# Performance work log

Measured on AMD Instinct MI355X. Metric: run time of the kernel, lower is better.

The kernel has to match this reference:

```python
import jax, jax.numpy as jnp
from jax import lax
import numpy as np

H = W = 768
N_BOXES = 512
C1, C2 = 32, 64
POOL = 5
NUM_CLASSES = 4
BN_EPS = 1e-5


def setup_inputs() -> dict:
    key = jax.random.key(0)
    ks = jax.random.split(key, 20)
    image = jax.random.normal(ks[0], (1, 3, H, W), jnp.float32)
    # valid boxes: xmax>xmin, ymax>ymin, inside [0, W)
    xmin = jax.random.randint(ks[1], (N_BOXES,), 0, W - 256)
    ymin = jax.random.randint(ks[2], (N_BOXES,), 0, H - 256)
    bw = jax.random.randint(ks[3], (N_BOXES,), 8, 256)
    bh = jax.random.randint(ks[4], (N_BOXES,), 8, 256)
    boxes = jnp.stack([xmin, ymin, xmin + bw, ymin + bh], axis=1).astype(jnp.int32)
    conv1_w = jax.random.normal(ks[5], (C1, 3, 3, 3), jnp.float32) * 0.1
    conv1_b = jax.random.normal(ks[6], (C1,), jnp.float32) * 0.01
    bn1_g = 1.0 + 0.1 * jax.random.normal(ks[7], (C1,), jnp.float32)
    bn1_b = 0.1 * jax.random.normal(ks[8], (C1,), jnp.float32)
    bn1_m = 0.1 * jax.random.normal(ks[9], (C1,), jnp.float32)
    bn1_v = jax.random.uniform(ks[10], (C1,), jnp.float32, 0.5, 1.5)
    conv2_w = jax.random.normal(ks[11], (C2, C1, 3, 3), jnp.float32) * 0.05
    conv2_b = jax.random.normal(ks[12], (C2,), jnp.float32) * 0.01
    bn2_g = 1.0 + 0.1 * jax.random.normal(ks[13], (C2,), jnp.float32)
    bn2_b = 0.1 * jax.random.normal(ks[14], (C2,), jnp.float32)
    bn2_m = 0.1 * jax.random.normal(ks[15], (C2,), jnp.float32)
    bn2_v = jax.random.uniform(ks[16], (C2,), jnp.float32, 0.5, 1.5)
    fc1_w = jax.random.normal(ks[17], (128, C2 * POOL * POOL), jnp.float32) * 0.02
    fc1_b = jnp.zeros((128,), jnp.float32)
    fc2_w = jax.random.normal(ks[18], (NUM_CLASSES, 128), jnp.float32) * 0.05
    fc2_b = jnp.zeros((NUM_CLASSES,), jnp.float32)
    return dict(image=image, boxes=boxes,
                conv1_w=conv1_w, conv1_b=conv1_b, bn1_g=bn1_g, bn1_b=bn1_b, bn1_m=bn1_m, bn1_v=bn1_v,
                conv2_w=conv2_w, conv2_b=conv2_b, bn2_g=bn2_g, bn2_b=bn2_b, bn2_m=bn2_m, bn2_v=bn2_v,
                fc1_w=fc1_w, fc1_b=fc1_b, fc2_w=fc2_w, fc2_b=fc2_b)


def _conv(x, w, b):
    y = lax.conv_general_dilated(x, w, (1, 1), ((1, 1), (1, 1)),
                                 dimension_numbers=("NCHW", "OIHW", "NCHW"))
    return y + b[None, :, None, None]


def _bn(x, g, b, m, v):
    scale = g / jnp.sqrt(v + BN_EPS)
    return x * scale[None, :, None, None] + (b - m * scale)[None, :, None, None]


def _forward(image, boxes, conv1_w, conv1_b, bn1_g, bn1_b, bn1_m, bn1_v,
             conv2_w, conv2_b, bn2_g, bn2_b, bn2_m, bn2_v,
             fc1_w, fc1_b, fc2_w, fc2_b):
    # backbone: Conv -> ReLU -> BN (order as in source), twice
    x = _bn(jax.nn.relu(_conv(image, conv1_w, conv1_b)), bn1_g, bn1_b, bn1_m, bn1_v)
    x = _bn(jax.nn.relu(_conv(x, conv2_w, conv2_b)), bn2_g, bn2_b, bn2_m, bn2_v)
    feat = x[0]  # [C2, H, W], batch assumed 1 as in the per-box slicing loop
    # integral image for exact adaptive-avg-pool over integer index rectangles
    integ = jnp.pad(feat, ((0, 0), (1, 0), (1, 0))).cumsum(1).cumsum(2)  # [C2,H+1,W+1]
    xmin, ymin, xmax, ymax = boxes[:, 0], boxes[:, 1], boxes[:, 2], boxes[:, 3]
    bh = ymax - ymin
    bw = xmax - xmin
    i = jnp.arange(POOL)
    # AdaptiveAvgPool2d bin edges: start=floor(i*L/5), end=ceil((i+1)*L/5)
    y0 = ymin[:, None] + (i * bh[:, None]) // POOL            # [N,5]
    y1 = ymin[:, None] + ((i + 1) * bh[:, None] + POOL - 1) // POOL
    x0 = xmin[:, None] + (i * bw[:, None]) // POOL
    x1 = xmin[:, None] + ((i + 1) * bw[:, None] + POOL - 1) // POOL

    def rect(ys, xs):  # [C2, N, 5, 5]
        return integ[:, ys[:, :, None], xs[:, None, :]]

    s = rect(y1, x1) - rect(y0, x1) - rect(y1, x0) + rect(y0, x0)
    area = ((y1 - y0)[:, :, None] * (x1 - x0)[:, None, :]).astype(feat.dtype)  # [N,5,5]
    pooled = s / area[None]                                    # [C2,N,5,5]
    flat = pooled.transpose(1, 0, 2, 3).reshape(boxes.shape[0], -1)  # [N, C2*25]
    h1 = jax.nn.relu(flat @ fc1_w.T + fc1_b)  # dropout is identity in eval
    return h1 @ fc2_w.T + fc2_b               # [N, num_classes]


def reference(image, boxes, conv1_w, conv1_b, bn1_g, bn1_b, bn1_m, bn1_v,
              conv2_w, conv2_b, bn2_g, bn2_b, bn2_m, bn2_v,
              fc1_w, fc1_b, fc2_w, fc2_b):
    return _forward(image, boxes, conv1_w, conv1_b, bn1_g, bn1_b, bn1_m, bn1_v,
                    conv2_w, conv2_b, bn2_g, bn2_b, bn2_m, bn2_v,
                    fc1_w, fc1_b, fc2_w, fc2_b)
```

## Files before the change

### kernel.cpp

```cpp
#include <hip/hip_runtime.h>
#include <hip/hip_bf16.h>

#define HH 768
#define WW 768
#define HWSZ (HH*WW)
#define BN_EPS 1e-5f
#define SEG 12
#define NSEG 64

typedef __attribute__((ext_vector_type(8))) short bf16x8;
typedef __attribute__((ext_vector_type(4))) float f32x4;

__device__ __forceinline__ float bf2f(unsigned short u) {
  union { unsigned int i; float f; } v; v.i = ((unsigned int)u) << 16; return v.f;
}
__device__ __forceinline__ unsigned short f2bf(float f) {
  union { float f; unsigned int i; } v; v.f = f;
  unsigned int x = v.i;
  return (unsigned short)((x + 0x7fffu + ((x >> 16) & 1u)) >> 16);
}
__device__ __forceinline__ float ldf(const void* p, int i, int flag) {
  return flag ? bf2f(((const unsigned short*)p)[i]) : ((const float*)p)[i];
}

#define DPP_ADD(v, CTRL) do {                                              \
    union { float f; int i; } _u; _u.f = (v);                              \
    int _t = __builtin_amdgcn_update_dpp(0, _u.i, (CTRL), 0xf, 0xf, true); \
    union { int i; float f; } _w; _w.i = _t;                               \
    (v) += _w.f;                                                           \
  } while (0)
__device__ __forceinline__ float row_prefix16(float v) {
  DPP_ADD(v, 0x111);
  DPP_ADD(v, 0x112);
  DPP_ADD(v, 0x114);
  DPP_ADD(v, 0x118);
  return v;
}

__global__ void k_prep(const void* __restrict__ c1b,
                       const void* __restrict__ g1, const void* __restrict__ b1,
                       const void* __restrict__ m1, const void* __restrict__ v1,
                       const void* __restrict__ c2b, const void* __restrict__ g2,
                       const void* __restrict__ b2, const void* __restrict__ m2,
                       const void* __restrict__ v2, const void* __restrict__ w1,
                       const void* __restrict__ fb1, const void* __restrict__ fw2,
                       const void* __restrict__ fb2,
                       int* __restrict__ flagp, float* __restrict__ cst)
{
  __shared__ int sflag;
  int tid = threadIdx.x;
  if (tid == 0) {
    const unsigned short* v1raw = (const unsigned short*)v1;
    int ok = 1;
    #pragma unroll
    for (int j = 0; j < 4; ++j) {
      unsigned short u = v1raw[2*j];
      if (u < 0x3E00u || u > 0x4040u) ok = 0;
    }
    sflag = ok;
    *flagp = ok;
  }
  __syncthreads();
  int flag = sflag;
  float* wc1   = cst;
  float* bias1 = cst + 864;
  float* sc1   = cst + 896;
  float* sh1   = cst + 928;
  float* bias2 = cst + 960;
  float* sc2   = cst + 1024;
  float* sh2   = cst + 1088;
  float* fb1c  = cst + 1152;
  float* w2c   = cst + 1280;
  float* fb2c  = cst + 1792;
  if (tid < 32) {
    float s = ldf(g1, tid, flag) * rsqrtf(ldf(v1, tid, flag) + BN_EPS);
    sc1[tid] = s;
    sh1[tid] = ldf(b1, tid, flag) - ldf(m1, tid, flag) * s;
    bias1[tid] = ldf(c1b, tid, flag);
  }
  if (tid < 64) {
    float s = ldf(g2, tid, flag) * rsqrtf(ldf(v2, tid, flag) + BN_EPS);
    sc2[tid] = s;
    sh2[tid] = ldf(b2, tid, flag) - ldf(m2, tid, flag) * s;
    bias2[tid] = ldf(c2b, tid, flag);
  }
  if (tid < 128) fb1c[tid] = ldf(fb1, tid, flag);
  if (tid < 4)   fb2c[tid] = ldf(fb2, tid, flag);
  for (int i = tid; i < 512; i += 256) w2c[i] = ldf(fw2, i, flag);
  for (int idx = tid; idx < 27*32; idx += 256) {
    int k = idx >> 5, co = idx & 31;
    wc1[idx] = ldf(w1, co*27 + k, flag);
  }
}

__global__ void k_a2(const void* __restrict__ w2, const int* __restrict__ flagp,
                     unsigned short* __restrict__ A2)
{
  int flag = *flagp;
  int idx = blockIdx.x * 256 + threadIdx.x;
  if (idx < 80*288) {
    int o = idx / 288, k = idx % 288, tap = k >> 5, ci = k & 31;
    A2[idx] = (o < 64) ? f2bf(ldf(w2, (o*32 + ci)*9 + tap, flag)) : (unsigned short)0;
  }
}

__global__ void k_cvtw1(unsigned short* __restrict__ dst, const void* __restrict__ src,
                        const int* __restrict__ flagp) {
  int flag = *flagp;
  for (int i = blockIdx.x * blockDim.x + threadIdx.x; i < 128*1600;
       i += gridDim.x * blockDim.x) {
    int t = i / 1600, r = i % 1600, cell = r >> 6, c = r & 63;
    dst[i] = f2bf(ldf(src, t*1600 + c*25 + cell, flag));
  }
}

__global__ __launch_bounds__(256) void k_conv1(const void* __restrict__ img,
    const int* __restrict__ flagp, const float* __restrict__ cst,
    unsigned short* __restrict__ feat1)
{
  const float* wc1   = cst;
  const float* bias1 = cst + 864;
  const float* sc1   = cst + 896;
  const float* sh1   = cst + 928;
  int flag = *flagp;
  __shared__ float tile[3][18][18];
  int tx = threadIdx.x, ty = threadIdx.y;
  int tid = ty * 16 + tx;
  int x0 = blockIdx.x * 16, y0 = blockIdx.y * 16;
  for (int idx = tid; idx < 3*18*18; idx += 256) {
    int ci = idx / 324, rem = idx % 324, r = rem / 18, cc = rem % 18;
    int gy = y0 - 1 + r, gx = x0 - 1 + cc;
    float v = 0.f;
    if (gy >= 0 && gy < HH && gx >= 0 && gx < WW)
      v = ldf(img, ci*HWSZ + gy*WW + gx, flag);
    tile[ci][r][cc] = v;
  }
  __syncthreads();
  float acc[32];
  #pragma unroll
  for (int c = 0; c < 32; ++c) acc[c] = 0.f;
  #pragma unroll
  for (int ci = 0; ci < 3; ++ci)
    #pragma unroll
    for (int ky = 0; ky < 3; ++ky)
      #pragma unroll
      for (int kx = 0; kx < 3; ++kx) {
        float v = tile[ci][ty + ky][tx + kx];
        const float* wr = wc1 + (ci*9 + ky*3 + kx) * 32;
        #pragma unroll
        for (int c = 0; c < 32; ++c) acc[c] += v * wr[c];
      }
  int gy = y0 + ty, gx = x0 + tx;
  unsigned short* dst = feat1 + (gy*WW + gx) * 32;
  #pragma unroll
  for (int g = 0; g < 4; ++g) {
    bf16x8 pack;
    #pragma unroll
    for (int e = 0; e < 8; ++e) {
      int c = g*8 + e;
      float r = fmaxf(acc[c] + bias1[c], 0.f);
      float f = r * sc1[c] + sh1[c];
      pack[e] = (short)f2bf(f);
    }
    *(bf16x8*)(dst + g*8) = pack;
  }
}

__global__ __launch_bounds__(256) void k_conv2t(const unsigned short* __restrict__ feat1,
    const unsigned short* __restrict__ A2, const float* __restrict__ cst,
    float* __restrict__ T)
{
  const float* bias2 = cst + 960;
  const float* sc2   = cst + 1024;
  const float* sh2   = cst + 1088;
  __shared__ unsigned short tile[14 * 34 * 40];
  int tid = threadIdx.x;
  int xb = blockIdx.x, ys = blockIdx.y;
  int x0 = xb * 32, ybase = ys * SEG;

  for (int idx = tid; idx < 14*34*4; idx += 256) {
    int q = idx & 3, p = (idx >> 2) % 34, r = idx / 136;
    int gy = ybase - 1 + r, gx = x0 - 1 + p;
    uint4 val = make_uint4(0u, 0u, 0u, 0u);
    if (gy >= 0 && gy < HH && gx >= 0 && gx < WW)
      val = *(const uint4*)(feat1 + (gy*WW + gx)*32 + q*8);
    *(uint4*)(tile + (r*34 + p)*40 + q*8) = val;
  }

  int w = tid >> 6, lane = tid & 63, quad = lane >> 4, l16 = lane & 15;
  int m = w * 16 + l16;
  bf16x8 afrag[9];
  #pragma unroll
  for (int t = 0; t < 9; ++t)
    afrag[t] = *(const bf16x8*)(A2 + m*288 + t*32 + quad*8);
  float bs[4], scv[4], shv[4];
  #pragma unroll
  for (int r = 0; r < 4; ++r) {
    int c = w*16 + quad*4 + r;
    bs[r] = bias2[c]; scv[r] = sc2[c]; shv[r] = sh2[c];
  }
  __syncthreads();

  f32x4 ys0 = (f32x4){0.f,0.f,0.f,0.f};
  f32x4 ys1 = (f32x4){0.f,0.f,0.f,0.f};
  int cbase = w*16 + quad*4;
  for (int dy = 0; dy < SEG; ++dy) {
    int y = ybase + dy;
    f32x4 acc[2];
    acc[0] = (f32x4){0.f,0.f,0.f,0.f};
    acc[1] = (f32x4){0.f,0.f,0.f,0.f};
    #pragma unroll
    for (int t = 0; t < 9; ++t) {
      int ky = t / 3, kx = t % 3;
      #pragma unroll
      for (int i = 0; i < 2; ++i) {
        int px = i*16 + l16 + kx;
        bf16x8 b = *(const bf16x8*)(tile + ((dy + ky)*34 + px)*40 + quad*8);
        acc[i] = __builtin_amdgcn_mfma_f32_16x16x32_bf16(afrag[t], b, acc[i], 0, 0, 0);
      }
    }
    #pragma unroll
    for (int r = 0; r < 4; ++r) {
      float v0 = fmaxf(acc[0][r] + bs[r], 0.f) * scv[r] + shv[r];
      float v1 = fmaxf(acc[1][r] + bs[r], 0.f) * scv[r] + shv[r];
      v0 = row_prefix16(v0);
      v1 = row_prefix16(v1);
      v1 += __shfl(v0, 15, 16);
      ys0[r] += v0;
      ys1[r] += v1;
    }
    *(f32x4*)(T + ((size_t)(y*WW + x0 + l16))*64 + cbase)      = ys0;
    *(f32x4*)(T + ((size_t)(y*WW + x0 + 16 + l16))*64 + cbase) = ys1;
  }
}

__global__ __launch_bounds__(64) void k_cgen_i(const float* __restrict__ T,
                                               float* __restrict__ C)
{
  int j = blockIdx.x, c = threadIdx.x;
  float run = 0.f;
  for (int i = 0; i < NSEG; ++i) {
    run += T[((size_t)((i*SEG + SEG-1)*WW + j*32 + 31))*64 + c];
    C[((size_t)(i*24 + j))*64 + c] = run;
  }
}
__global__ __launch_bounds__(64) void k_cgen_j(float* __restrict__ C)
{
  int i = blockIdx.x, c = threadIdx.x;
  float run = 0.f;
  #pragma unroll
  for (int j = 0; j < 24; ++j) {
    size_t idx = ((size_t)(i*24 + j))*64 + c;
    run += C[idx];
    C[idx] = run;
  }
}

__global__ __launch_bounds__(256) void k_ab(const float* __restrict__ T,
    const float* __restrict__ C, float* __restrict__ A, float* __restrict__ Bp)
{
  int part = blockIdx.y, tid = threadIdx.x;
  int c = tid & 63, s = tid >> 6;
  if (part == 0) {
    int y = blockIdx.x * 4 + s;
    float run = 0.f;
    #pragma unroll
    for (int j = 0; j < 24; ++j) {
      run += T[((size_t)(y*WW + j*32 + 31))*64 + c];
      A[((size_t)(y*24 + j))*64 + c] = run;
    }
  } else {
    int x = blockIdx.x * 4 + s;
    int j = x >> 5;
    float run = 0.f;
    for (int i = 0; i < NSEG; ++i) {
      run += T[((size_t)((i*SEG + SEG-1)*WW + x))*64 + c];
      float cj = (j > 0) ? C[((size_t)(i*24 + (j-1)))*64 + c] : 0.f;
      Bp[((size_t)(i*WW + x))*64 + c] = run + cj;
    }
  }
}

__device__ __forceinline__ float icorner(const float* __restrict__ T,
    const float* __restrict__ A, const float* __restrict__ Bp,
    int c, int yy, int xx)
{
  int i = yy / SEG, j = xx >> 5;
  float v = T[((size_t)(yy*WW + xx))*64 + c];
  if (j > 0) v += A[((size_t)(yy*24 + (j-1)))*64 + c];
  if (i > 0) v += Bp[((size_t)((i-1)*WW + xx))*64 + c];
  return v;
}

__global__ __launch_bounds__(256) void k_roi3(const float* __restrict__ T,
    const float* __restrict__ A, const float* __restrict__ Bp,
    const int* __restrict__ boxes, float* __restrict__ flat)
{
  int b = blockIdx.x;
  int xmin = boxes[b*4 + 0], ymin = boxes[b*4 + 1];
  int xmax = boxes[b*4 + 2], ymax = boxes[b*4 + 3];
  int bh = ymax - ymin, bw = xmax - xmin;
  for (int idx = threadIdx.x; idx < 1600; idx += 256) {
    int c = idx & 63, cell = idx >> 6, i = cell / 5, j = cell % 5;
    int y0 = ymin + (i*bh)/5,  y1 = ymin + ((i+1)*bh + 4)/5;
    int x0 = xmin + (j*bw)/5,  x1 = xmin + ((j+1)*bw + 4)/5;
    float s = icorner(T, A, Bp, c, y1-1, x1-1);
    if (y0 > 0)           s -= icorner(T, A, Bp, c, y0-1, x1-1);
    if (x0 > 0)           s -= icorner(T, A, Bp, c, y1-1, x0-1);
    if (y0 > 0 && x0 > 0) s += icorner(T, A, Bp, c, y0-1, x0-1);
    float area = (float)((y1 - y0) * (x1 - x0));
    flat[b*1600 + cell*64 + c] = s / area;
  }
}

__global__ __launch_bounds__(256) void k_conv2_c16(const unsigned short* __restrict__ feat1,
    const unsigned short* __restrict__ A2, const float* __restrict__ cst,
    float* __restrict__ chunk, int c0, int cnw)
{
  const float* bias2 = cst + 960;
  const float* sc2   = cst + 1024;
  const float* sh2   = cst + 1088;
  __shared__ unsigned short tile[3 * 130 * 40];
  int tid = threadIdx.x;
  int y = blockIdx.y, x0 = blockIdx.x * 128;
  for (int idx = tid; idx < 3*130*4; idx += 256) {
    int q = idx & 3, p = (idx >> 2) % 130, r = idx / 520;
    int gy = y - 1 + r, gx = x0 - 1 + p;
    uint4 val = make_uint4(0u, 0u, 0u, 0u);
    if (gy >= 0 && gy < HH && gx >= 0 && gx < WW)
      val = *(const uint4*)(feat1 + (gy*WW + gx)*32 + q*8);
    *(uint4*)(tile + (r*130 + p)*40 + q*8) = val;
  }
  __syncthreads();
  int w = tid >> 6, lane = tid & 63, quad = lane >> 4, l16 = lane & 15;
  int m = c0 + l16;
  f32x4 acc[2];
  acc[0] = (f32x4){0.f,0.f,0.f,0.f};
  acc[1] = (f32x4){0.f,0.f,0.f,0.f};
  #pragma unroll
  for (int t = 0; t < 9; ++t) {
    int ky = t / 3, kx = t % 3;
    bf16x8 a = *(const bf16x8*)(A2 + m*288 + t*32 + quad*8);
    #pragma unroll
    for (int i = 0; i < 2; ++i) {
      int px = w*32 + i*16 + l16 + kx;
      bf16x8 b = *(const bf16x8*)(tile + (ky*130 + px)*40 + quad*8);
      acc[i] = __builtin_amdgcn_mfma_f32_16x16x32_bf16(a, b, acc[i], 0, 0, 0);
    }
  }
  #pragma unroll
  for (int r = 0; r < 4; ++r) {
    int cl = quad*4 + r;
    if (cl < cnw) {
      int c = c0 + cl;
      float bsv = bias2[c], s = sc2[c], sh = sh2[c];
      float* dst = chunk + cl*HWSZ + y*WW;
      #pragma unroll
      for (int i = 0; i < 2; ++i) {
        float v = fmaxf(acc[i][r] + bsv, 0.f) * s + sh;
        dst[x0 + w*32 + i*16 + l16] = v;
      }
    }
  }
}
__global__ __launch_bounds__(256) void k_csy(float* __restrict__ buf) {
  int t = blockIdx.x * 256 + threadIdx.x;
  int c = t / WW, x = t % WW;
  float* p = buf + c*HWSZ + x;
  float run = 0.f;
  for (int yb = 0; yb < HH; yb += 16) {
    float v[16];
    #pragma unroll
    for (int j = 0; j < 16; ++j) v[j] = p[(yb + j) * WW];
    #pragma unroll
    for (int j = 0; j < 16; ++j) { run += v[j]; v[j] = run; }
    #pragma unroll
    for (int j = 0; j < 16; ++j) p[(yb + j) * WW] = v[j];
  }
}
__global__ __launch_bounds__(256) void k_csx(float* __restrict__ buf) {
  int row = blockIdx.x * 4 + (threadIdx.x >> 6);
  int lane = threadIdx.x & 63;
  float* p = buf + (long)row * WW;
  float carry = 0.f;
  for (int ch = 0; ch < 12; ++ch) {
    float v = p[ch*64 + lane];
    #pragma unroll
    for (int off = 1; off < 64; off <<= 1) {
      float t = __shfl_up(v, off);
      v = (lane >= off) ? v + t : v;
    }
    v += carry;
    p[ch*64 + lane] = v;
    carry = __shfl(v, 63);
  }
}
__global__ __launch_bounds__(256) void k_roi(const float* __restrict__ integ,
    const int* __restrict__ boxes, float* __restrict__ flat, int c0, int cn)
{
  int b = blockIdx.x;
  int xmin = boxes[b*4 + 0], ymin = boxes[b*4 + 1];
  int xmax = boxes[b*4 + 2], ymax = boxes[b*4 + 3];
  int bh = ymax - ymin, bw = xmax - xmin;
  for (int idx = threadIdx.x; idx < cn*25; idx += 256) {
    int cl = idx / 25, cell = idx % 25, i = cell / 5, j = cell % 5;
    int y0 = ymin + (i*bh)/5,      y1 = ymin + ((i+1)*bh + 4)/5;
    int x0 = xmin + (j*bw)/5,      x1 = xmin + ((j+1)*bw + 4)/5;
    const float* I = integ + cl*HWSZ;
    float a  = I[(y1-1)*WW + (x1-1)];
    float bl = (y0 > 0) ? I[(y0-1)*WW + (x1-1)] : 0.f;
    float cr = (x0 > 0) ? I[(y1-1)*WW + (x0-1)] : 0.f;
    float d  = (y0 > 0 && x0 > 0) ? I[(y0-1)*WW + (x0-1)] : 0.f;
    float s = a - bl - cr + d;
    float area = (float)((y1 - y0) * (x1 - x0));
    flat[b*1600 + cell*64 + (c0 + cl)] = s / area;
  }
}

__global__ __launch_bounds__(128) void k_fc(const float* __restrict__ flat,
    const unsigned short* __restrict__ w1c, const float* __restrict__ cst,
    const int* __restrict__ flagp, void* __restrict__ out)
{
  const float* fb1c = cst + 1152;
  const float* w2c  = cst + 1280;
  const float* fb2c = cst + 1792;
  __shared__ float sf[1600];
  __shared__ float hbuf[128];
  int b = blockIdx.x, t = threadIdx.x;
  for (int i = t; i < 1600; i += 128) sf[i] = flat[b*1600 + i];
  __syncthreads();
  float a = fb1c[t];
  const unsigned short* wr = w1c + t * 1600;
  for (int k = 0; k < 1600; k += 8) {
    bf16x8 wv = *(const bf16x8*)(wr + k);
    #pragma unroll
    for (int e = 0; e < 8; ++e)
      a += sf[k + e] * bf2f((unsigned short)wv[e]);
  }
  hbuf[t] = fmaxf(a, 0.f);
  __syncthreads();
  if (t < 4) {
    float a2 = fb2c[t];
    for (int k = 0; k < 128; ++k) a2 += hbuf[k] * w2c[t*128 + k];
    if (*flagp) ((unsigned short*)out)[b*4 + t] = f2bf(a2);
    else        ((float*)out)[b*4 + t] = a2;
  }
}

extern "C" void kernel_launch(void* const* d_in, const int* in_sizes, int n_in,
                              void* d_out, int out_size, void* d_ws, size_t ws_size,
                              hipStream_t stream) {
  const void* img = d_in[0];
  const int* boxes = (const int*)d_in[1];
  const void* c1w = d_in[2];  const void* c1b = d_in[3];
  const void* g1  = d_in[4];  const void* b1  = d_in[5];
  const void* m1  = d_in[6];  const void* v1  = d_in[7];
  const void* c2w = d_in[8];  const void* c2b = d_in[9];
  const void* g2  = d_in[10]; const void* b2  = d_in[11];
  const void* m2  = d_in[12]; const void* v2  = d_in[13];
  const void* fw1 = d_in[14]; const void* fb1 = d_in[15];
  const void* fw2 = d_in[16]; const void* fb2 = d_in[17];

  char* ws = (char*)d_ws;
  unsigned short* A2 = (unsigned short*)ws;
  float* cst = (float*)(ws + 46080);
  int* flag = (int*)(ws + 53264);
  unsigned short* w1c  = (unsigned short*)(ws + 3592224);
  float* flat = (float*)(ws + 4001824);
  unsigned short* feat1 = (unsigned short*)(ws + 7278624);
  float* T = (float*)(ws + 45027360);
  float* Aarr = (float*)(ws + 7278624);
  float* Bparr = Aarr + (size_t)768*24*64;
  float* Carr = Bparr + (size_t)NSEG*768*64;

  const size_t base = 45027360;
  int cn;
  if      (ws_size >= base + 64ull*HWSZ*4) cn = 64;
  else if (ws_size >= base + 16ull*HWSZ*4) cn = 16;
  else if (ws_size >= base +  8ull*HWSZ*4) cn = 8;
  else if (ws_size >= base +  4ull*HWSZ*4) cn = 4;
  else if (ws_size >= base +  2ull*HWSZ*4) cn = 2;
  else                                     cn = 1;

  hipLaunchKernelGGL(k_prep, dim3(1), dim3(256), 0, stream,
                     c1b, g1, b1, m1, v1, c2b, g2, b2, m2, v2, c1w,
                     fb1, fw2, fb2, flag, cst);
  hipLaunchKernelGGL(k_a2, dim3(90), dim3(256), 0, stream, c2w, flag, A2);
  hipLaunchKernelGGL(k_cvtw1, dim3(128), dim3(256), 0, stream, w1c, fw1, flag);
  hipLaunchKernelGGL(k_conv1, dim3(48, 48), dim3(16, 16), 0, stream,
                     img, flag, cst, feat1);

  if (cn == 64) {
    hipLaunchKernelGGL(k_conv2t, dim3(24, NSEG), dim3(256), 0, stream,
                       feat1, A2, cst, T);
    hipLaunchKernelGGL(k_cgen_i, dim3(24), dim3(64), 0, stream, T, Carr);
    hipLaunchKernelGGL(k_cgen_j, dim3(NSEG), dim3(64), 0, stream, Carr);
    hipLaunchKernelGGL(k_ab, dim3(192, 2), dim3(256), 0, stream, T, Carr, Aarr, Bparr);
    hipLaunchKernelGGL(k_roi3, dim3(512), dim3(256), 0, stream,
                       T, Aarr, Bparr, boxes, flat);
  } else {
    for (int c0 = 0; c0 < 64; c0 += cn) {
      hipLaunchKernelGGL(k_conv2_c16, dim3(6, 768), dim3(256), 0, stream,
                         feat1, A2, cst, T, c0, cn);
      hipLaunchKernelGGL(k_csy, dim3(cn*3), dim3(256), 0, stream, T);
      hipLaunchKernelGGL(k_csx, dim3(cn*192), dim3(256), 0, stream, T);
      hipLaunchKernelGGL(k_roi, dim3(512), dim3(256), 0, stream, T, boxes, flat, c0, cn);
    }
  }
  hipLaunchKernelGGL(k_fc, dim3(512), dim3(128), 0, stream, flat, w1c, cst, flag,
                     d_out);
}
```

Measured before the change: 247.4 us.

## Move conv1 and FC1 to MFMA, merge prep kernels, shrink segment height

Conv1 becomes a bf16 MFMA GEMM over a packed 3-channel tile, and the first FC layer becomes an MFMA kernel that handles 16 boxes per block, with pooled features now stored as bf16. The three weight-prep kernels are merged into one multi-block launch. The conv2 segment height drops from 12 to 8 rows (96 segments) to raise parallelism, and the column-carry generation is split across four wave groups. Together these aim to cut launch count and serial scalar FMA work, at the cost of bf16 rounding on the image, conv1 inputs and pooled features, plus more carry segments to scan.

```diff
diff --git a/kernel.cpp b/kernel.cpp
--- a/kernel.cpp
+++ b/kernel.cpp
@@ -5,8 +5,8 @@
 #define WW 768
 #define HWSZ (HH*WW)
 #define BN_EPS 1e-5f
-#define SEG 12
-#define NSEG 64
+#define SEG 8
+#define NSEG 96
 
 typedef __attribute__((ext_vector_type(8))) short bf16x8;
 typedef __attribute__((ext_vector_type(4))) float f32x4;
@@ -37,6 +37,17 @@
   return v;
 }
 
+__device__ __forceinline__ int detect_flag(const void* v1) {
+  const unsigned short* v1raw = (const unsigned short*)v1;
+  int ok = 1;
+  #pragma unroll
+  for (int j = 0; j < 4; ++j) {
+    unsigned short u = v1raw[2*j];
+    if (u < 0x3E00u || u > 0x4040u) ok = 0;
+  }
+  return ok;
+}
+
 __global__ void k_prep(const void* __restrict__ c1b,
                        const void* __restrict__ g1, const void* __restrict__ b1,
                        const void* __restrict__ m1, const void* __restrict__ v1,
@@ -44,125 +55,135 @@
                        const void* __restrict__ b2, const void* __restrict__ m2,
                        const void* __restrict__ v2, const void* __restrict__ w1,
                        const void* __restrict__ fb1, const void* __restrict__ fw2,
-                       const void* __restrict__ fb2,
-                       int* __restrict__ flagp, float* __restrict__ cst)
-{
-  __shared__ int sflag;
-  int tid = threadIdx.x;
-  if (tid == 0) {
-    const unsigned short* v1raw = (const unsigned short*)v1;
-    int ok = 1;
-    #pragma unroll
-    for (int j = 0; j < 4; ++j) {
-      unsigned short u = v1raw[2*j];
-      if (u < 0x3E00u || u > 0x4040u) ok = 0;
-    }
-    sflag = ok;
-    *flagp = ok;
-  }
-  __syncthreads();
-  int flag = sflag;
-  float* wc1   = cst;
-  float* bias1 = cst + 864;
-  float* sc1   = cst + 896;
-  float* sh1   = cst + 928;
-  float* bias2 = cst + 960;
-  float* sc2   = cst + 1024;
-  float* sh2   = cst + 1088;
-  float* fb1c  = cst + 1152;
-  float* w2c   = cst + 1280;
-  float* fb2c  = cst + 1792;
-  if (tid < 32) {
-    float s = ldf(g1, tid, flag) * rsqrtf(ldf(v1, tid, flag) + BN_EPS);
-    sc1[tid] = s;
-    sh1[tid] = ldf(b1, tid, flag) - ldf(m1, tid, flag) * s;
-    bias1[tid] = ldf(c1b, tid, flag);
-  }
-  if (tid < 64) {
-    float s = ldf(g2, tid, flag) * rsqrtf(ldf(v2, tid, flag) + BN_EPS);
-    sc2[tid] = s;
-    sh2[tid] = ldf(b2, tid, flag) - ldf(m2, tid, flag) * s;
-    bias2[tid] = ldf(c2b, tid, flag);
-  }
-  if (tid < 128) fb1c[tid] = ldf(fb1, tid, flag);
-  if (tid < 4)   fb2c[tid] = ldf(fb2, tid, flag);
-  for (int i = tid; i < 512; i += 256) w2c[i] = ldf(fw2, i, flag);
-  for (int idx = tid; idx < 27*32; idx += 256) {
-    int k = idx >> 5, co = idx & 31;
-    wc1[idx] = ldf(w1, co*27 + k, flag);
-  }
-}
-
-__global__ void k_a2(const void* __restrict__ w2, const int* __restrict__ flagp,
-                     unsigned short* __restrict__ A2)
-{
-  int flag = *flagp;
-  int idx = blockIdx.x * 256 + threadIdx.x;
-  if (idx < 80*288) {
-    int o = idx / 288, k = idx % 288, tap = k >> 5, ci = k & 31;
-    A2[idx] = (o < 64) ? f2bf(ldf(w2, (o*32 + ci)*9 + tap, flag)) : (unsigned short)0;
-  }
-}
-
-__global__ void k_cvtw1(unsigned short* __restrict__ dst, const void* __restrict__ src,
-                        const int* __restrict__ flagp) {
-  int flag = *flagp;
-  for (int i = blockIdx.x * blockDim.x + threadIdx.x; i < 128*1600;
-       i += gridDim.x * blockDim.x) {
+                       const void* __restrict__ fb2, const void* __restrict__ w2,
+                       const void* __restrict__ fw1,
+                       int* __restrict__ flagp, float* __restrict__ cst,
+                       unsigned short* __restrict__ A2, unsigned short* __restrict__ A1,
+                       unsigned short* __restrict__ w1c)
+{
+  int flag = detect_flag(v1);
+  int tid = threadIdx.x, bid = blockIdx.x;
+  int gid = bid * 256 + tid;
+
+  if (bid == 0) {
+    if (tid == 0) *flagp = flag;
+    float* bias1 = cst + 864;
+    float* sc1   = cst + 896;
+    float* sh1   = cst + 928;
+    float* bias2 = cst + 960;
+    float* sc2   = cst + 1024;
+    float* sh2   = cst + 1088;
+    float* fb1c  = cst + 1152;
+    float* w2c   = cst + 1280;
+    float* fb2c  = cst + 1792;
+    if (tid < 32) {
+      float s = ldf(g1, tid, flag) * rsqrtf(ldf(v1, tid, flag) + BN_EPS);
+      sc1[tid] = s;
+      sh1[tid] = ldf(b1, tid, flag) - ldf(m1, tid, flag) * s;
+      bias1[tid] = ldf(c1b, tid, flag);
+    }
+    if (tid < 64) {
+      float s = ldf(g2, tid, flag) * rsqrtf(ldf(v2, tid, flag) + BN_EPS);
+      sc2[tid] = s;
+      sh2[tid] = ldf(b2, tid, flag) - ldf(m2, tid, flag) * s;
+      bias2[tid] = ldf(c2b, tid, flag);
+    }
+    if (tid < 128) fb1c[tid] = ldf(fb1, tid, flag);
+    if (tid < 4)   fb2c[tid] = ldf(fb2, tid, flag);
+    for (int i = tid; i < 512; i += 256) w2c[i] = ldf(fw2, i, flag);
+  }
+  if (gid < 80*288) {
+    int o = gid / 288, k = gid % 288, tap = k >> 5, ci = k & 31;
+    A2[gid] = (o < 64) ? f2bf(ldf(w2, (o*32 + ci)*9 + tap, flag)) : (unsigned short)0;
+  }
+  if (gid < 32*64) {
+    int o = gid >> 6, k = gid & 63, tap = k >> 2, ci = k & 3;
+    A1[gid] = (tap < 9 && ci < 3) ? f2bf(ldf(w1, o*27 + ci*9 + tap, flag))
+                                  : (unsigned short)0;
+  }
+  for (int i = gid; i < 128*1600; i += 128*256) {
     int t = i / 1600, r = i % 1600, cell = r >> 6, c = r & 63;
-    dst[i] = f2bf(ldf(src, t*1600 + c*25 + cell, flag));
-  }
-}
-
-__global__ __launch_bounds__(256) void k_conv1(const void* __restrict__ img,
-    const int* __restrict__ flagp, const float* __restrict__ cst,
-    unsigned short* __restrict__ feat1)
-{
-  const float* wc1   = cst;
+    w1c[i] = f2bf(ldf(fw1, t*1600 + c*25 + cell, flag));
+  }
+}
+
+__global__ __launch_bounds__(256) void k_conv1m(const void* __restrict__ img,
+    const int* __restrict__ flagp, const unsigned short* __restrict__ A1,
+    const float* __restrict__ cst, unsigned short* __restrict__ feat1)
+{
   const float* bias1 = cst + 864;
   const float* sc1   = cst + 896;
   const float* sh1   = cst + 928;
   int flag = *flagp;
-  __shared__ float tile[3][18][18];
-  int tx = threadIdx.x, ty = threadIdx.y;
-  int tid = ty * 16 + tx;
-  int x0 = blockIdx.x * 16, y0 = blockIdx.y * 16;
-  for (int idx = tid; idx < 3*18*18; idx += 256) {
-    int ci = idx / 324, rem = idx % 324, r = rem / 18, cc = rem % 18;
-    int gy = y0 - 1 + r, gx = x0 - 1 + cc;
-    float v = 0.f;
-    if (gy >= 0 && gy < HH && gx >= 0 && gx < WW)
-      v = ldf(img, ci*HWSZ + gy*WW + gx, flag);
-    tile[ci][r][cc] = v;
-  }
+  __shared__ unsigned short tile[18 * 34 * 4];
+  int tid = threadIdx.x;
+  int x0 = blockIdx.x * 32, ybase = blockIdx.y * 16;
+
+  for (int idx = tid; idx < 18*34; idx += 256) {
+    int r = idx / 34, p = idx % 34;
+    int gy = ybase - 1 + r, gx = x0 - 1 + p;
+    unsigned short e0 = 0, e1 = 0, e2 = 0;
+    if (gy >= 0 && gy < HH && gx >= 0 && gx < WW) {
+      e0 = f2bf(ldf(img, 0*HWSZ + gy*WW + gx, flag));
+      e1 = f2bf(ldf(img, 1*HWSZ + gy*WW + gx, flag));
+      e2 = f2bf(ldf(img, 2*HWSZ + gy*WW + gx, flag));
+    }
+    ushort4 pk; pk.x = e0; pk.y = e1; pk.z = e2; pk.w = 0;
+    *(ushort4*)(tile + idx*4) = pk;
+  }
+
+  int w = tid >> 6, lane = tid & 63, quad = lane >> 4, l16 = lane & 15;
+  bf16x8 a1f[2][2];
+  #pragma unroll
+  for (int mt = 0; mt < 2; ++mt)
+    #pragma unroll
+    for (int kt = 0; kt < 2; ++kt)
+      a1f[mt][kt] = *(const bf16x8*)(A1 + (mt*16 + l16)*64 + kt*32 + quad*8);
+  int t0 = 2*quad, t1 = 2*quad + 1;
+  int ky0 = t0/3, kx0 = t0%3, ky1 = t1/3, kx1 = t1%3;
   __syncthreads();
-  float acc[32];
-  #pragma unroll
-  for (int c = 0; c < 32; ++c) acc[c] = 0.f;
-  #pragma unroll
-  for (int ci = 0; ci < 3; ++ci)
-    #pragma unroll
-    for (int ky = 0; ky < 3; ++ky)
+
+  for (int dyw = 0; dyw < 4; ++dyw) {
+    int dy = dyw*4 + w;
+    int y = ybase + dy;
+    f32x4 acc[2][2];
+    #pragma unroll
+    for (int mt = 0; mt < 2; ++mt)
       #pragma unroll
-      for (int kx = 0; kx < 3; ++kx) {
-        float v = tile[ci][ty + ky][tx + kx];
-        const float* wr = wc1 + (ci*9 + ky*3 + kx) * 32;
-        #pragma unroll
-        for (int c = 0; c < 32; ++c) acc[c] += v * wr[c];
+      for (int i = 0; i < 2; ++i)
+        acc[mt][i] = (f32x4){0.f,0.f,0.f,0.f};
+    #pragma unroll
+    for (int i = 0; i < 2; ++i) {
+      int pxb = i*16 + l16;
+      union { uint2 u[2]; bf16x8 v; } b0;
+      b0.u[0] = *(const uint2*)(tile + ((dy + ky0)*34 + pxb + kx0)*4);
+      b0.u[1] = *(const uint2*)(tile + ((dy + ky1)*34 + pxb + kx1)*4);
+      union { uint2 u[2]; bf16x8 v; } b1v;
+      b1v.u[0] = *(const uint2*)(tile + ((dy + 2)*34 + pxb + 2)*4);
+      b1v.u[1] = make_uint2(0u, 0u);
+      #pragma unroll
+      for (int mt = 0; mt < 2; ++mt) {
+        acc[mt][i] = __builtin_amdgcn_mfma_f32_16x16x32_bf16(a1f[mt][0], b0.v, acc[mt][i], 0, 0, 0);
+        acc[mt][i] = __builtin_amdgcn_mfma_f32_16x16x32_bf16(a1f[mt][1], b1v.v, acc[mt][i], 0, 0, 0);
       }
-  int gy = y0 + ty, gx = x0 + tx;
-  unsigned short* dst = feat1 + (gy*WW + gx) * 32;
-  #pragma unroll
-  for (int g = 0; g < 4; ++g) {
-    bf16x8 pack;
-    #pragma unroll
-    for (int e = 0; e < 8; ++e) {
-      int c = g*8 + e;
-      float r = fmaxf(acc[c] + bias1[c], 0.f);
-      float f = r * sc1[c] + sh1[c];
-      pack[e] = (short)f2bf(f);
-    }
-    *(bf16x8*)(dst + g*8) = pack;
+    }
+    #pragma unroll
+    for (int mt = 0; mt < 2; ++mt) {
+      int cb = mt*16 + quad*4;
+      float bs0 = bias1[cb], bs1 = bias1[cb+1], bs2 = bias1[cb+2], bs3 = bias1[cb+3];
+      float s0 = sc1[cb], s1 = sc1[cb+1], s2 = sc1[cb+2], s3 = sc1[cb+3];
+      float h0 = sh1[cb], h1 = sh1[cb+1], h2 = sh1[cb+2], h3 = sh1[cb+3];
+      #pragma unroll
+      for (int i = 0; i < 2; ++i) {
+        int px = x0 + i*16 + l16;
+        ushort4 pk;
+        pk.x = f2bf(fmaxf(acc[mt][i][0] + bs0, 0.f) * s0 + h0);
+        pk.y = f2bf(fmaxf(acc[mt][i][1] + bs1, 0.f) * s1 + h1);
+        pk.z = f2bf(fmaxf(acc[mt][i][2] + bs2, 0.f) * s2 + h2);
+        pk.w = f2bf(fmaxf(acc[mt][i][3] + bs3, 0.f) * s3 + h3);
+        *(ushort4*)(feat1 + ((size_t)(y*WW + px))*32 + cb) = pk;
+      }
+    }
   }
 }
 
@@ -173,12 +194,12 @@
   const float* bias2 = cst + 960;
   const float* sc2   = cst + 1024;
   const float* sh2   = cst + 1088;
-  __shared__ unsigned short tile[14 * 34 * 40];
+  __shared__ unsigned short tile[10 * 34 * 40];
   int tid = threadIdx.x;
   int xb = blockIdx.x, ys = blockIdx.y;
   int x0 = xb * 32, ybase = ys * SEG;
 
-  for (int idx = tid; idx < 14*34*4; idx += 256) {
+  for (int idx = tid; idx < 10*34*4; idx += 256) {
     int q = idx & 3, p = (idx >> 2) % 34, r = idx / 136;
     int gy = ybase - 1 + r, gx = x0 - 1 + p;
     uint4 val = make_uint4(0u, 0u, 0u, 0u);
@@ -234,14 +255,28 @@
   }
 }
 
-__global__ __launch_bounds__(64) void k_cgen_i(const float* __restrict__ T,
-                                               float* __restrict__ C)
-{
-  int j = blockIdx.x, c = threadIdx.x;
+__global__ __launch_bounds__(256) void k_cgen_i(const float* __restrict__ T,
+                                                float* __restrict__ C)
+{
+  int j = blockIdx.x;
+  int c = threadIdx.x & 63, g = threadIdx.x >> 6;
+  __shared__ float gtot[4][64];
   float run = 0.f;
-  for (int i = 0; i < NSEG; ++i) {
+  #pragma unroll 4
+  for (int ii = 0; ii < 24; ++ii) {
+    int i = g*24 + ii;
     run += T[((size_t)((i*SEG + SEG-1)*WW + j*32 + 31))*64 + c];
     C[((size_t)(i*24 + j))*64 + c] = run;
+  }
+  gtot[g][c] = run;
+  __syncthreads();
+  if (g > 0) {
+    float off = 0.f;
+    for (int gg = 0; gg < g; ++gg) off += gtot[gg][c];
+    for (int ii = 0; ii < 24; ++ii) {
+      int i = g*24 + ii;
+      C[((size_t)(i*24 + j))*64 + c] += off;
+    }
   }
 }
 __global__ __launch_bounds__(64) void k_cgen_j(float* __restrict__ C)
@@ -273,6 +308,7 @@
     int x = blockIdx.x * 4 + s;
     int j = x >> 5;
     float run = 0.f;
+    #pragma unroll 4
     for (int i = 0; i < NSEG; ++i) {
       run += T[((size_t)((i*SEG + SEG-1)*WW + x))*64 + c];
       float cj = (j > 0) ? C[((size_t)(i*24 + (j-1)))*64 + c] : 0.f;
@@ -285,7 +321,7 @@
     const float* __restrict__ A, const float* __restrict__ Bp,
     int c, int yy, int xx)
 {
-  int i = yy / SEG, j = xx >> 5;
+  int i = yy >> 3, j = xx >> 5;
   float v = T[((size_t)(yy*WW + xx))*64 + c];
   if (j > 0) v += A[((size_t)(yy*24 + (j-1)))*64 + c];
   if (i > 0) v += Bp[((size_t)((i-1)*WW + xx))*64 + c];
@@ -294,7 +330,7 @@
 
 __global__ __launch_bounds__(256) void k_roi3(const float* __restrict__ T,
     const float* __restrict__ A, const float* __restrict__ Bp,
-    const int* __restrict__ boxes, float* __restrict__ flat)
+    const int* __restrict__ boxes, unsigned short* __restrict__ flat)
 {
   int b = blockIdx.x;
   int xmin = boxes[b*4 + 0], ymin = boxes[b*4 + 1];
@@ -309,7 +345,53 @@
     if (x0 > 0)           s -= icorner(T, A, Bp, c, y1-1, x0-1);
     if (y0 > 0 && x0 > 0) s += icorner(T, A, Bp, c, y0-1, x0-1);
     float area = (float)((y1 - y0) * (x1 - x0));
-    flat[b*1600 + cell*64 + c] = s / area;
+    flat[b*1600 + cell*64 + c] = f2bf(s / area);
+  }
+}
+
+__global__ __launch_bounds__(256) void k_fcm(const unsigned short* __restrict__ flat,
+    const unsigned short* __restrict__ w1c, const float* __restrict__ cst,
+    const int* __restrict__ flagp, void* __restrict__ out)
+{
+  const float* fb1c = cst + 1152;
+  const float* w2c  = cst + 1280;
+  const float* fb2c = cst + 1792;
+  __shared__ unsigned short sflat[16 * 1608];
+  __shared__ float hbuf[16 * 132];
+  int tid = threadIdx.x;
+  int b0 = blockIdx.x * 16;
+  for (int ii = tid; ii < 3200; ii += 256) {
+    int bi = ii / 200, ch = ii % 200;
+    *(uint4*)(sflat + bi*1608 + ch*8) = *(const uint4*)(flat + (b0 + bi)*1600 + ch*8);
+  }
+  __syncthreads();
+  int w = tid >> 6, lane = tid & 63, quad = lane >> 4, l16 = lane & 15;
+  f32x4 acc[2];
+  acc[0] = (f32x4){0.f,0.f,0.f,0.f};
+  acc[1] = (f32x4){0.f,0.f,0.f,0.f};
+  for (int kt = 0; kt < 50; ++kt) {
+    bf16x8 b = *(const bf16x8*)(sflat + l16*1608 + kt*32 + quad*8);
+    #pragma unroll
+    for (int mt = 0; mt < 2; ++mt) {
+      bf16x8 a = *(const bf16x8*)(w1c + ((w*2 + mt)*16 + l16)*1600 + kt*32 + quad*8);
+      acc[mt] = __builtin_amdgcn_mfma_f32_16x16x32_bf16(a, b, acc[mt], 0, 0, 0);
+    }
+  }
+  #pragma unroll
+  for (int mt = 0; mt < 2; ++mt) {
+    #pragma unroll
+    for (int r = 0; r < 4; ++r) {
+      int h = (w*2 + mt)*16 + quad*4 + r;
+      hbuf[l16*132 + h] = fmaxf(acc[mt][r] + fb1c[h], 0.f);
+    }
+  }
+  __syncthreads();
+  if (tid < 64) {
+    int bi = tid >> 2, o = tid & 3;
+    float a2 = fb2c[o];
+    for (int k = 0; k < 128; ++k) a2 += hbuf[bi*132 + k] * w2c[o*128 + k];
+    if (*flagp) ((unsigned short*)out)[(b0 + bi)*4 + o] = f2bf(a2);
+    else        ((float*)out)[(b0 + bi)*4 + o] = a2;
   }
 }
 
@@ -396,7 +478,7 @@
   }
 }
 __global__ __launch_bounds__(256) void k_roi(const float* __restrict__ integ,
-    const int* __restrict__ boxes, float* __restrict__ flat, int c0, int cn)
+    const int* __restrict__ boxes, unsigned short* __restrict__ flat, int c0, int cn)
 {
   int b = blockIdx.x;
   int xmin = boxes[b*4 + 0], ymin = boxes[b*4 + 1];
@@ -413,37 +495,7 @@
     float d  = (y0 > 0 && x0 > 0) ? I[(y0-1)*WW + (x0-1)] : 0.f;
     float s = a - bl - cr + d;
     float area = (float)((y1 - y0) * (x1 - x0));
-    flat[b*1600 + cell*64 + (c0 + cl)] = s / area;
-  }
-}
-
-__global__ __launch_bounds__(128) void k_fc(const float* __restrict__ flat,
-    const unsigned short* __restrict__ w1c, const float* __restrict__ cst,
-    const int* __restrict__ flagp, void* __restrict__ out)
-{
-  const float* fb1c = cst + 1152;
-  const float* w2c  = cst + 1280;
-  const float* fb2c = cst + 1792;
-  __shared__ float sf[1600];
-  __shared__ float hbuf[128];
-  int b = blockIdx.x, t = threadIdx.x;
-  for (int i = t; i < 1600; i += 128) sf[i] = flat[b*1600 + i];
-  __syncthreads();
-  float a = fb1c[t];
-  const unsigned short* wr = w1c + t * 1600;
-  for (int k = 0; k < 1600; k += 8) {
-    bf16x8 wv = *(const bf16x8*)(wr + k);
-    #pragma unroll
-    for (int e = 0; e < 8; ++e)
-      a += sf[k + e] * bf2f((unsigned short)wv[e]);
-  }
-  hbuf[t] = fmaxf(a, 0.f);
-  __syncthreads();
-  if (t < 4) {
-    float a2 = fb2c[t];
-    for (int k = 0; k < 128; ++k) a2 += hbuf[k] * w2c[t*128 + k];
-    if (*flagp) ((unsigned short*)out)[b*4 + t] = f2bf(a2);
-    else        ((float*)out)[b*4 + t] = a2;
+    flat[b*1600 + cell*64 + (c0 + cl)] = f2bf(s / area);
   }
 }
 
@@ -463,10 +515,11 @@
 
   char* ws = (char*)d_ws;
   unsigned short* A2 = (unsigned short*)ws;
-  float* cst = (float*)(ws + 46080);
-  int* flag = (int*)(ws + 53264);
+  unsigned short* A1 = (unsigned short*)(ws + 46080);
+  float* cst = (float*)(ws + 50176);
+  int* flag = (int*)(ws + 57360);
   unsigned short* w1c  = (unsigned short*)(ws + 3592224);
-  float* flat = (float*)(ws + 4001824);
+  unsigned short* flat = (unsigned short*)(ws + 4001824);
   unsigned short* feat1 = (unsigned short*)(ws + 7278624);
   float* T = (float*)(ws + 45027360);
   float* Aarr = (float*)(ws + 7278624);
@@ -482,18 +535,16 @@
   else if (ws_size >= base +  2ull*HWSZ*4) cn = 2;
   else                                     cn = 1;
 
-  hipLaunchKernelGGL(k_prep, dim3(1), dim3(256), 0, stream,
+  hipLaunchKernelGGL(k_prep, dim3(128), dim3(256), 0, stream,
                      c1b, g1, b1, m1, v1, c2b, g2, b2, m2, v2, c1w,
-                     fb1, fw2, fb2, flag, cst);
-  hipLaunchKernelGGL(k_a2, dim3(90), dim3(256), 0, stream, c2w, flag, A2);
-  hipLaunchKernelGGL(k_cvtw1, dim3(128), dim3(256), 0, stream, w1c, fw1, flag);
-  hipLaunchKernelGGL(k_conv1, dim3(48, 48), dim3(16, 16), 0, stream,
-                     img, flag, cst, feat1);
+                     fb1, fw2, fb2, c2w, fw1, flag, cst, A2, A1, w1c);
+  hipLaunchKernelGGL(k_conv1m, dim3(24, 48), dim3(256), 0, stream,
+                     img, flag, A1, cst, feat1);
 
   if (cn == 64) {
     hipLaunchKernelGGL(k_conv2t, dim3(24, NSEG), dim3(256), 0, stream,
                        feat1, A2, cst, T);
-    hipLaunchKernelGGL(k_cgen_i, dim3(24), dim3(64), 0, stream, T, Carr);
+    hipLaunchKernelGGL(k_cgen_i, dim3(24), dim3(256), 0, stream, T, Carr);
     hipLaunchKernelGGL(k_cgen_j, dim3(NSEG), dim3(64), 0, stream, Carr);
     hipLaunchKernelGGL(k_ab, dim3(192, 2), dim3(256), 0, stream, T, Carr, Aarr, Bparr);
     hipLaunchKernelGGL(k_roi3, dim3(512), dim3(256), 0, stream,
@@ -507,6 +558,6 @@
       hipLaunchKernelGGL(k_roi, dim3(512), dim3(256), 0, stream, T, boxes, flat, c0, cn);
     }
   }
-  hipLaunchKernelGGL(k_fc, dim3(512), dim3(128), 0, stream, flat, w1c, cst, flag,
+  hipLaunchKernelGGL(k_fcm, dim3(32), dim3(256), 0, stream, flat, w1c, cst, flag,
                      d_out);
 }
```

Measured after the change: 225.3 us. 8.9% less time.
